# Kernel optimization log

Measured on AMD Instinct MI355X. Metric: run time of the kernel, lower is better.

## Reference

```python
import jax, jax.numpy as jnp
import numpy as np

N = 20000      # nodes
IN = 256       # in_dim
OUT = 128      # out_dim
S = 8          # num_sect
K = S + 1      # sectors + self branch
EP = 40000     # edges per sector


def setup_inputs() -> dict:
    key = jax.random.key(0)
    ks = jax.random.split(key, 10)
    x = jax.random.normal(ks[0], (N, IN), jnp.float32)
    rows = jax.random.randint(ks[1], (S, EP), 0, N)  # src (adj row)
    cols = jax.random.randint(ks[2], (S, EP), 0, N)  # dst (adj col)
    # degree norms (buffers derived from the graph, as in compute_norm)
    out_deg = np.bincount(np.asarray(rows).ravel(), minlength=N).astype(np.float32)
    in_deg = np.bincount(np.asarray(cols).ravel(), minlength=N).astype(np.float32)
    out_norm = jnp.asarray(np.clip(out_deg, 1.0, None) ** -0.5)[:, None]  # [N,1]
    in_norm = jnp.asarray(np.clip(in_deg, 1.0, None) ** -0.5)[:, None]    # [N,1]
    s = 0.05  # xavier-ish scale
    W_self = jax.random.normal(ks[3], (IN, OUT), jnp.float32) * s
    W_sect = jax.random.normal(ks[4], (S, IN, OUT), jnp.float32) * s
    WC = jax.random.normal(ks[5], (OUT, OUT), jnp.float32) * s
    WD = jax.random.normal(ks[6], (OUT, OUT), jnp.float32) * s
    gate_w = jax.random.normal(ks[7], (2 * K * OUT, 1), jnp.float32) * s
    gate_b = jnp.zeros((1,), jnp.float32)
    return {"x": x, "W_self": W_self, "W_sect": W_sect, "WC": WC, "WD": WD,
            "gate_w": gate_w, "gate_b": gate_b, "out_norm": out_norm,
            "in_norm": in_norm, "rows": rows, "cols": cols}


def reference(x, W_self, W_sect, WC, WD, gate_w, gate_b, out_norm, in_norm, rows, cols):
    n = x.shape[0]
    # --- forward_sector_agg (dropout is identity in eval / drop_rate=0) ---
    z_self = x @ W_self                                    # [N, OUT]
    H = jnp.einsum('ni,sio->sno', x, W_sect) * out_norm    # [S, N, OUT]
    def agg(h, r, c):  # sparse adj @ h : z[src] += h[dst]
        return jax.ops.segment_sum(h[c], r, num_segments=n)
    Z = jax.vmap(agg)(H, rows, cols)                       # [S, N, OUT]
    z = jnp.concatenate([z_self[None], Z], axis=0)         # [K, N, OUT]
    z = jnp.transpose(z, (1, 0, 2)) * in_norm[:, :, None]  # [N, K, OUT]
    # --- heter_sen_interaction ---
    zc = z @ WC                                            # [N, K, D]
    com = jnp.einsum('nkd,njd->nkj', zc, zc)
    ac = jax.nn.softmax(com, axis=2)
    z_com = jnp.einsum('nkj,njd->nkd', ac, zc).reshape(n, -1)
    zd = z @ WD
    sub = zd[:, :, None, :] - zd[:, None, :, :]            # [N, K, K, D]
    ds = jnp.einsum('nkd,nkjd->nkj', zd, sub)
    ad = jax.nn.softmax(ds, axis=2)
    z_dis = jnp.einsum('nkj,nkjd->nkd', ad, sub).reshape(n, -1)
    cat = jnp.concatenate([z_com, z_dis], axis=-1)         # [N, 2*K*D]
    beta = jax.nn.sigmoid(cat @ gate_w + gate_b)           # [N, 1]
    return beta * z_com + (1.0 - beta) * z_dis             # [N, K*D]
```

## Files before the change

kernel.cpp:

```cpp
#include <hip/hip_runtime.h>
#include <math.h>

#define N_NODES 20000
#define IN_DIM  256
#define OUT_DIM 128
#define S_SECT  8
#define K_BR    9
#define NK      (K_BR*OUT_DIM)
#define EP_EDGE 40000
#define N_EDGES (S_SECT*EP_EDGE)
#define N_BINS  (S_SECT*N_NODES)
#define SCAN_BLOCKS 160
#define M_ROWS  (N_NODES*K_BR)
#define ZP      136

typedef float v4f __attribute__((ext_vector_type(4)));
typedef short v8s __attribute__((ext_vector_type(8)));

__device__ inline unsigned short f2bf(float f) {
  union { float f; unsigned u; } v; v.f = f;
  unsigned r = v.u + 0x7fff + ((v.u >> 16) & 1);
  return (unsigned short)(r >> 16);
}
__device__ inline float bf2f(unsigned short h) {
  union { unsigned u; float f; } v; v.u = ((unsigned)h) << 16;
  return v.f;
}

__global__ __launch_bounds__(256) void k_prep_wt(
    const float* __restrict__ Wself, const float* __restrict__ Wsect,
    unsigned short* __restrict__ Wtg)
{
  const int id = blockIdx.x * 256 + threadIdx.x;
  if (id >= NK*IN_DIM) return;
  const int j = id >> 8, k = id & 255;
  float w;
  if (j < OUT_DIM) w = Wself[(size_t)k*OUT_DIM + j];
  else {
    const int s = (j - OUT_DIM) >> 7, c = (j - OUT_DIM) & 127;
    w = Wsect[(size_t)s*(IN_DIM*OUT_DIM) + (size_t)k*OUT_DIM + c];
  }
  Wtg[id] = f2bf(w);
}

__global__ __launch_bounds__(256) void k_prep_xbf(
    const float* __restrict__ x, unsigned short* __restrict__ xbf)
{
  const int id = blockIdx.x * 256 + threadIdx.x;
  if (id >= N_NODES*IN_DIM/4) return;
  const float4 v = ((const float4*)x)[id];
  uint2 o;
  o.x = (unsigned)f2bf(v.x) | ((unsigned)f2bf(v.y) << 16);
  o.y = (unsigned)f2bf(v.z) | ((unsigned)f2bf(v.w) << 16);
  ((uint2*)xbf)[id] = o;
}

__global__ __launch_bounds__(256, 4) void k_gemm_xw_mfma(
    const unsigned short* __restrict__ xbf, const unsigned short* __restrict__ Wtg,
    const float* __restrict__ outn, const float* __restrict__ inn,
    unsigned short* __restrict__ Hbuf, unsigned short* __restrict__ Zbufh)
{
  __shared__ unsigned short Bls[128*ZP];
  const int t = threadIdx.x;
  const int wave = t >> 6, lane = t & 63;
  const int mrow = lane & 15, quad = lane >> 4;
  const int m0 = blockIdx.x * 128 + wave * 32;
  const int jbase = blockIdx.y * 128;

  v4f acc[2][8];
  #pragma unroll
  for (int rb = 0; rb < 2; ++rb)
    #pragma unroll
    for (int jt = 0; jt < 8; ++jt) acc[rb][jt] = (v4f){0.f,0.f,0.f,0.f};

  for (int kh = 0; kh < 2; ++kh) {
    #pragma unroll
    for (int i = 0; i < 8; ++i) {
      const int idx = t + i*256;
      const int row = idx >> 4, c8 = idx & 15;
      *(uint4*)(Bls + row*ZP + c8*8) =
          *(const uint4*)(Wtg + (size_t)(jbase + row)*IN_DIM + kh*128 + c8*8);
    }
    v8s afr[2][4];
    #pragma unroll
    for (int rb = 0; rb < 2; ++rb) {
      const int r = m0 + rb*16 + mrow;
      const bool ok = (r < N_NODES);
      const unsigned short* src = xbf + (size_t)r*IN_DIM + kh*128 + quad*8;
      #pragma unroll
      for (int kq = 0; kq < 4; ++kq) {
        v8s f = {0,0,0,0,0,0,0,0};
        if (ok) f = *(const v8s*)(src + kq*32);
        afr[rb][kq] = f;
      }
    }
    __syncthreads();

    #pragma unroll
    for (int kq = 0; kq < 4; ++kq) {
      #pragma unroll
      for (int jt = 0; jt < 8; ++jt) {
        const v8s bf = *(const v8s*)(Bls + (jt*16 + mrow)*ZP + kq*32 + quad*8);
        acc[0][jt] = __builtin_amdgcn_mfma_f32_16x16x32_bf16(afr[0][kq], bf, acc[0][jt], 0, 0, 0);
        acc[1][jt] = __builtin_amdgcn_mfma_f32_16x16x32_bf16(afr[1][kq], bf, acc[1][jt], 0, 0, 0);
      }
    }
    __syncthreads();
  }

  if (blockIdx.y == 0) {
    #pragma unroll
    for (int rb = 0; rb < 2; ++rb)
      #pragma unroll
      for (int p = 0; p < 4; ++p) {
        const int R = m0 + rb*16 + quad*4 + p;
        if (R >= N_NODES) continue;
        const float iw = inn[R];
        #pragma unroll
        for (int jt = 0; jt < 8; ++jt)
          Zbufh[(size_t)R*NK + jt*16 + mrow] = f2bf(acc[rb][jt][p] * iw);
      }
  } else {
    const int s = blockIdx.y - 1;
    #pragma unroll
    for (int rb = 0; rb < 2; ++rb)
      #pragma unroll
      for (int p = 0; p < 4; ++p) {
        const int R = m0 + rb*16 + quad*4 + p;
        if (R >= N_NODES) continue;
        const float ow = outn[R];
        #pragma unroll
        for (int jt = 0; jt < 8; ++jt)
          Hbuf[((size_t)s*N_NODES + R)*OUT_DIM + jt*16 + mrow] = f2bf(acc[rb][jt][p] * ow);
      }
  }
}

__global__ __launch_bounds__(256) void k_count(
    const int* __restrict__ rows, int* __restrict__ cnt)
{
  const int id = blockIdx.x * 256 + threadIdx.x;
  if (id >= N_EDGES) return;
  const int s = id / EP_EDGE;
  atomicAdd(&cnt[s * N_NODES + rows[id]], 1);
}

__global__ __launch_bounds__(256) void k_scan1(
    const int* __restrict__ cnt, int* __restrict__ bsum)
{
  __shared__ int sh[256];
  const int t = threadIdx.x;
  const int base = blockIdx.x * 1000;
  int s = 0;
  if (t < 250) {
    const int i = base + t*4;
    s = cnt[i] + cnt[i+1] + cnt[i+2] + cnt[i+3];
  }
  sh[t] = s; __syncthreads();
  for (int off = 128; off > 0; off >>= 1) {
    if (t < off) sh[t] += sh[t + off];
    __syncthreads();
  }
  if (t == 0) bsum[blockIdx.x] = sh[0];
}

__global__ void k_scan2(const int* __restrict__ bsum, int* __restrict__ boff)
{
  if (threadIdx.x == 0) {
    int acc = 0;
    for (int b = 0; b < SCAN_BLOCKS; ++b) { boff[b] = acc; acc += bsum[b]; }
  }
}

__global__ __launch_bounds__(256) void k_scan3(
    const int* __restrict__ cnt, const int* __restrict__ boff,
    int* __restrict__ offs)
{
  __shared__ int sh[256];
  const int t = threadIdx.x;
  const int base = blockIdx.x * 1000;
  int v[4] = {0,0,0,0};
  int mySum = 0;
  if (t < 250) {
    const int i = base + t*4;
    v[0]=cnt[i]; v[1]=cnt[i+1]; v[2]=cnt[i+2]; v[3]=cnt[i+3];
    mySum = v[0]+v[1]+v[2]+v[3];
  }
  sh[t] = mySum; __syncthreads();
  for (int off = 1; off < 256; off <<= 1) {
    int add = (t >= off) ? sh[t - off] : 0;
    __syncthreads();
    sh[t] += add;
    __syncthreads();
  }
  if (t < 250) {
    int excl = boff[blockIdx.x] + sh[t] - mySum;
    const int i = base + t*4;
    offs[i]   = excl;           excl += v[0];
    offs[i+1] = excl;           excl += v[1];
    offs[i+2] = excl;           excl += v[2];
    offs[i+3] = excl;
  }
}

__global__ __launch_bounds__(256) void k_scatter(
    const int* __restrict__ rows, const int* __restrict__ cols,
    const int* __restrict__ offs, int* __restrict__ cur,
    int* __restrict__ eCol)
{
  const int id = blockIdx.x * 256 + threadIdx.x;
  if (id >= N_EDGES) return;
  const int s = id / EP_EDGE;
  const int bin = s * N_NODES + rows[id];
  const int pos = offs[bin] + atomicAdd(&cur[bin], 1);
  eCol[pos] = cols[id];
}

__global__ __launch_bounds__(256) void k_agg_csr(
    const unsigned short* __restrict__ Hbuf, const int* __restrict__ offs,
    const int* __restrict__ cnt, const int* __restrict__ eCol,
    const float* __restrict__ inn, unsigned short* __restrict__ Zbufh)
{
  const long long tid = (long long)blockIdx.x * 256 + threadIdx.x;
  const int group = (int)(tid >> 5);
  if (group >= N_BINS) return;
  const int lane = (int)(tid & 31);
  const int s = group / N_NODES;
  const int r = group - s * N_NODES;
  const int start = offs[group];
  const int n = cnt[group];
  float4 acc = {0.f, 0.f, 0.f, 0.f};
  for (int i = 0; i < n; ++i) {
    const int c = eCol[start + i];
    const uint2 h = *(const uint2*)(Hbuf + ((size_t)s*N_NODES + c)*OUT_DIM + lane*4);
    acc.x += bf2f((unsigned short)h.x);
    acc.y += bf2f((unsigned short)(h.x >> 16));
    acc.z += bf2f((unsigned short)h.y);
    acc.w += bf2f((unsigned short)(h.y >> 16));
  }
  const float w = inn[r];
  uint2 o;
  o.x = (unsigned)f2bf(acc.x * w) | ((unsigned)f2bf(acc.y * w) << 16);
  o.y = (unsigned)f2bf(acc.z * w) | ((unsigned)f2bf(acc.w * w) << 16);
  *(uint2*)(Zbufh + ((size_t)r*K_BR + 1 + s)*OUT_DIM + lane*4) = o;
}

__global__ __launch_bounds__(256) void k_prep_bt(
    const float* __restrict__ WC, const float* __restrict__ WD,
    unsigned short* __restrict__ Btg)
{
  const int id = blockIdx.x * 256 + threadIdx.x;
  const int n = id >> 7, k = id & 127;
  const float w = (n < OUT_DIM) ? WC[k*OUT_DIM + n] : WD[k*OUT_DIM + (n - OUT_DIM)];
  Btg[id] = f2bf(w);
}

__global__ __launch_bounds__(256, 4) void k_gemm_zcd(
    const unsigned short* __restrict__ Zbufh, const unsigned short* __restrict__ Btg,
    unsigned short* __restrict__ ZCD)
{
  __shared__ unsigned short Bls[128*ZP];
  const int t = threadIdx.x;
  const int wave = t >> 6, lane = t & 63;
  const int m0 = blockIdx.x * 128 + wave * 32;
  const int mrow = lane & 15, quad = lane >> 4;

  v8s afr[2][4];
  #pragma unroll
  for (int rb = 0; rb < 2; ++rb) {
    const int r = m0 + rb*16 + mrow;
    const bool ok = (r < M_ROWS);
    const unsigned short* src = Zbufh + (size_t)r*OUT_DIM + quad*8;
    #pragma unroll
    for (int kq = 0; kq < 4; ++kq) {
      v8s f = {0,0,0,0,0,0,0,0};
      if (ok) f = *(const v8s*)(src + kq*32);
      afr[rb][kq] = f;
    }
  }

  for (int jh = 0; jh < 2; ++jh) {
    #pragma unroll
    for (int i = 0; i < 8; ++i) {
      const int idx = t + i*256;
      const int row = idx >> 4, c8 = idx & 15;
      *(uint4*)(Bls + row*ZP + c8*8) =
          *(const uint4*)(Btg + (size_t)(jh*128 + row)*OUT_DIM + c8*8);
    }
    __syncthreads();

    v4f acc[2][8];
    #pragma unroll
    for (int rb = 0; rb < 2; ++rb)
      #pragma unroll
      for (int j = 0; j < 8; ++j) acc[rb][j] = (v4f){0.f,0.f,0.f,0.f};

    #pragma unroll
    for (int j = 0; j < 8; ++j) {
      const unsigned short* bp = Bls + (j*16 + mrow)*ZP + quad*8;
      #pragma unroll
      for (int kq = 0; kq < 4; ++kq) {
        const v8s bf = *(const v8s*)(bp + kq*32);
        acc[0][j] = __builtin_amdgcn_mfma_f32_16x16x32_bf16(afr[0][kq], bf, acc[0][j], 0, 0, 0);
        acc[1][j] = __builtin_amdgcn_mfma_f32_16x16x32_bf16(afr[1][kq], bf, acc[1][j], 0, 0, 0);
      }
    }

    unsigned short* Z = ZCD + (size_t)jh * N_NODES * NK;
    #pragma unroll
    for (int rb = 0; rb < 2; ++rb)
      #pragma unroll
      for (int p = 0; p < 4; ++p) {
        const int R = m0 + rb*16 + quad*4 + p;
        if (R >= M_ROWS) continue;
        const int node = R / 9, kk = R - node*9;
        const size_t base = (size_t)node*NK + kk*OUT_DIM;
        #pragma unroll
        for (int j = 0; j < 8; ++j)
          Z[base + j*16 + mrow] = f2bf(acc[rb][j][p]);
      }
    __syncthreads();
  }
}

__global__ __launch_bounds__(256) void k_interact3(
    const unsigned short* __restrict__ ZCD,
    const float* __restrict__ gw, const float* __restrict__ gb,
    float* __restrict__ out)
{
  __shared__ float graw[8][2][K_BR][10];
  __shared__ float gs[8][2][K_BR][10];
  __shared__ float redw[2][2];
  const int t  = threadIdx.x;
  const int n0 = blockIdx.x * 8;

  {
    const int wv = t >> 6, lane = t & 63;
    const int r = lane & 15, quad = lane >> 4;
    #pragma unroll
    for (int q = 0; q < 4; ++q) {
      const int idx = wv*4 + q;
      const int node = idx >> 1, mat = idx & 1;
      const unsigned short* src = ZCD + (size_t)mat*N_NODES*NK
                                  + (size_t)(n0+node)*NK + (size_t)r*OUT_DIM + quad*8;
      v8s frag[4];
      #pragma unroll
      for (int kq = 0; kq < 4; ++kq) {
        v8s f = {0,0,0,0,0,0,0,0};
        if (r < K_BR) f = *(const v8s*)(src + kq*32);
        frag[kq] = f;
      }
      v4f acc = {0.f,0.f,0.f,0.f};
      #pragma unroll
      for (int kq = 0; kq < 4; ++kq)
        acc = __builtin_amdgcn_mfma_f32_16x16x32_bf16(frag[kq], frag[kq], acc, 0, 0, 0);
      if (r < K_BR) {
        #pragma unroll
        for (int p = 0; p < 4; ++p) {
          const int m = quad*4 + p;
          if (m < K_BR) graw[node][mat][m][r] = acc[p];
        }
      }
    }
  }
  __syncthreads();

  if (t < 144) {
    const int node = t / 18;
    const int rem  = t - node*18;
    const int mat  = (rem >= 9) ? 1 : 0;
    const int k    = rem - mat*9;
    float v[9];
    if (mat == 0) {
      #pragma unroll
      for (int j = 0; j < 9; ++j) v[j] = graw[node][0][k][j];
    } else {
      const float gkk = graw[node][1][k][k];
      #pragma unroll
      for (int j = 0; j < 9; ++j) v[j] = gkk - graw[node][1][k][j];
    }
    float m = v[0];
    #pragma unroll
    for (int j = 1; j < 9; ++j) m = fmaxf(m, v[j]);
    float sum = 0.f;
    #pragma unroll
    for (int j = 0; j < 9; ++j) { v[j] = expf(v[j] - m); sum += v[j]; }
    const float inv = 1.f / sum;
    #pragma unroll
    for (int j = 0; j < 9; ++j) gs[node][mat][k][j] = v[j] * inv;
  }
  __syncthreads();

  const int half = t >> 7;
  const int d    = t & 127;
  const int wh   = (t >> 6) & 1;
  const int lane = t & 63;
  const float gbv = gb[0];
  float gwc[9], gwd[9];
  #pragma unroll
  for (int j = 0; j < 9; ++j) {
    gwc[j] = gw[j*OUT_DIM + d];
    gwd[j] = gw[NK + j*OUT_DIM + d];
  }

  for (int nn = 0; nn < 4; ++nn) {
    const int node = half*4 + nn;
    const unsigned short* zcp = ZCD + (size_t)(n0+node)*NK + d;
    const unsigned short* zdp = zcp + (size_t)N_NODES*NK;
    float zcj[9], zdj[9];
    #pragma unroll
    for (int j = 0; j < 9; ++j) {
      zcj[j] = bf2f(zcp[j*OUT_DIM]);
      zdj[j] = bf2f(zdp[j*OUT_DIM]);
    }
    float zcomK[9], zdisK[9];
    float gp = 0.f;
    #pragma unroll
    for (int k = 0; k < 9; ++k) {
      float zc = 0.f, ad = 0.f;
      #pragma unroll
      for (int j = 0; j < 9; ++j) {
        zc += gs[node][0][k][j] * zcj[j];
        ad += gs[node][1][k][j] * zdj[j];
      }
      zcomK[k] = zc;
      zdisK[k] = zdj[k] - ad;
      gp += zc * gwc[k] + zdisK[k] * gwd[k];
    }
    #pragma unroll
    for (int off = 32; off > 0; off >>= 1) gp += __shfl_down(gp, off, 64);
    if (lane == 0) redw[half][wh] = gp;
    __syncthreads();
    const float beta = 1.f / (1.f + expf(-(redw[half][0] + redw[half][1] + gbv)));
    #pragma unroll
    for (int k = 0; k < 9; ++k)
      out[(size_t)(n0+node)*NK + k*OUT_DIM + d] = beta*zcomK[k] + (1.f-beta)*zdisK[k];
    __syncthreads();
  }
}

extern "C" void kernel_launch(void* const* d_in, const int* in_sizes, int n_in,
                              void* d_out, int out_size, void* d_ws, size_t ws_size,
                              hipStream_t stream)
{
  const float* x     = (const float*)d_in[0];
  const float* Wself = (const float*)d_in[1];
  const float* Wsect = (const float*)d_in[2];
  const float* WC    = (const float*)d_in[3];
  const float* WD    = (const float*)d_in[4];
  const float* gw    = (const float*)d_in[5];
  const float* gb    = (const float*)d_in[6];
  const float* outn  = (const float*)d_in[7];
  const float* inn   = (const float*)d_in[8];
  const int*   rows  = (const int*)d_in[9];
  const int*   cols  = (const int*)d_in[10];
  float* out = (float*)d_out;

  char* p = (char*)d_ws;
  unsigned short* Hbuf  = (unsigned short*)p; p += (size_t)S_SECT*N_NODES*OUT_DIM*2;
  unsigned short* Zbufh = (unsigned short*)p; p += (size_t)M_ROWS*OUT_DIM*2;
  unsigned short* ZCD   = (unsigned short*)p; p += (size_t)2*N_NODES*NK*2;
  int* cnt    = (int*)p;                      p += (size_t)N_BINS*4;
  int* offs   = (int*)p;                      p += (size_t)N_BINS*4;
  int* cur    = (int*)p;                      p += (size_t)N_BINS*4;
  int* bsum   = (int*)p;                      p += 256*4;
  int* boff   = (int*)p;                      p += 256*4;
  int* eCol   = (int*)p;                      p += (size_t)N_EDGES*4;
  unsigned short* Btg = (unsigned short*)p;   p += 256*128*2;
  unsigned short* Wtg = (unsigned short*)p;   p += (size_t)NK*IN_DIM*2;
  unsigned short* xbf = (unsigned short*)p;   p += (size_t)N_NODES*IN_DIM*2;

  hipMemsetAsync(cnt, 0, (size_t)N_BINS*4, stream);
  hipMemsetAsync(cur, 0, (size_t)N_BINS*4, stream);

  k_prep_wt<<<(NK*IN_DIM + 255)/256, 256, 0, stream>>>(Wself, Wsect, Wtg);
  k_prep_bt<<<128, 256, 0, stream>>>(WC, WD, Btg);
  k_prep_xbf<<<(N_NODES*IN_DIM/4 + 255)/256, 256, 0, stream>>>(x, xbf);

  dim3 gA((N_NODES + 127)/128, K_BR);
  k_gemm_xw_mfma<<<gA, 256, 0, stream>>>(xbf, Wtg, outn, inn, Hbuf, Zbufh);

  const int eb = (N_EDGES + 255)/256;
  k_count  <<<eb, 256, 0, stream>>>(rows, cnt);
  k_scan1  <<<SCAN_BLOCKS, 256, 0, stream>>>(cnt, bsum);
  k_scan2  <<<1, 64, 0, stream>>>(bsum, boff);
  k_scan3  <<<SCAN_BLOCKS, 256, 0, stream>>>(cnt, boff, offs);
  k_scatter<<<eb, 256, 0, stream>>>(rows, cols, offs, cur, eCol);

  const int aggBlocks = (N_BINS*32 + 255)/256;
  k_agg_csr<<<aggBlocks, 256, 0, stream>>>(Hbuf, offs, cnt, eCol, inn, Zbufh);

  k_gemm_zcd<<<(M_ROWS + 127)/128, 256, 0, stream>>>(Zbufh, Btg, ZCD);

  k_interact3<<<N_NODES/8, 256, 0, stream>>>(ZCD, gw, gb, out);
}
```

Before: 323.2 us.

## Fuse prep kernels, convert x in-GEMM, and stage ZCD tiles in LDS for interaction

Merges the two weight-prep kernels into one launch and drops the separate x-to-bf16 kernel: the first GEMM now loads fp32 x directly and converts it in registers. The GEMM is retiled to 64 rows per block, with each block covering three 128-column output slices, so the A fragment is loaded once and reused. The interaction kernel saves the ZCD fragments it already loads into LDS and reads them from there, instead of reloading them from global memory. The cost is fewer blocks in the first GEMM, a larger LDS footprint in the interaction kernel (lower occupancy), and repeated Wtg tile loads per block.

```diff
diff --git a/kernel.cpp b/kernel.cpp
--- a/kernel.cpp
+++ b/kernel.cpp
@@ -13,6 +13,7 @@
 #define SCAN_BLOCKS 160
 #define M_ROWS  (N_NODES*K_BR)
 #define ZP      136
+#define TP      136
 
 typedef float v4f __attribute__((ext_vector_type(4)));
 typedef short v8s __attribute__((ext_vector_type(8)));
@@ -27,36 +28,33 @@
   return v.f;
 }
 
-__global__ __launch_bounds__(256) void k_prep_wt(
+__global__ __launch_bounds__(256) void k_prep(
     const float* __restrict__ Wself, const float* __restrict__ Wsect,
-    unsigned short* __restrict__ Wtg)
+    const float* __restrict__ WC, const float* __restrict__ WD,
+    unsigned short* __restrict__ Wtg, unsigned short* __restrict__ Btg)
 {
   const int id = blockIdx.x * 256 + threadIdx.x;
-  if (id >= NK*IN_DIM) return;
-  const int j = id >> 8, k = id & 255;
-  float w;
-  if (j < OUT_DIM) w = Wself[(size_t)k*OUT_DIM + j];
-  else {
-    const int s = (j - OUT_DIM) >> 7, c = (j - OUT_DIM) & 127;
-    w = Wsect[(size_t)s*(IN_DIM*OUT_DIM) + (size_t)k*OUT_DIM + c];
-  }
-  Wtg[id] = f2bf(w);
-}
-
-__global__ __launch_bounds__(256) void k_prep_xbf(
-    const float* __restrict__ x, unsigned short* __restrict__ xbf)
-{
-  const int id = blockIdx.x * 256 + threadIdx.x;
-  if (id >= N_NODES*IN_DIM/4) return;
-  const float4 v = ((const float4*)x)[id];
-  uint2 o;
-  o.x = (unsigned)f2bf(v.x) | ((unsigned)f2bf(v.y) << 16);
-  o.y = (unsigned)f2bf(v.z) | ((unsigned)f2bf(v.w) << 16);
-  ((uint2*)xbf)[id] = o;
+  if (id < NK*IN_DIM) {
+    const int j = id >> 8, k = id & 255;
+    float w;
+    if (j < OUT_DIM) w = Wself[(size_t)k*OUT_DIM + j];
+    else {
+      const int s = (j - OUT_DIM) >> 7, c = (j - OUT_DIM) & 127;
+      w = Wsect[(size_t)s*(IN_DIM*OUT_DIM) + (size_t)k*OUT_DIM + c];
+    }
+    Wtg[id] = f2bf(w);
+  } else {
+    const int id2 = id - NK*IN_DIM;
+    if (id2 < 256*128) {
+      const int n = id2 >> 7, k = id2 & 127;
+      const float w = (n < OUT_DIM) ? WC[k*OUT_DIM + n] : WD[k*OUT_DIM + (n - OUT_DIM)];
+      Btg[id2] = f2bf(w);
+    }
+  }
 }
 
 __global__ __launch_bounds__(256, 4) void k_gemm_xw_mfma(
-    const unsigned short* __restrict__ xbf, const unsigned short* __restrict__ Wtg,
+    const float* __restrict__ x, const unsigned short* __restrict__ Wtg,
     const float* __restrict__ outn, const float* __restrict__ inn,
     unsigned short* __restrict__ Hbuf, unsigned short* __restrict__ Zbufh)
 {
@@ -64,75 +62,79 @@
   const int t = threadIdx.x;
   const int wave = t >> 6, lane = t & 63;
   const int mrow = lane & 15, quad = lane >> 4;
-  const int m0 = blockIdx.x * 128 + wave * 32;
-  const int jbase = blockIdx.y * 128;
-
-  v4f acc[2][8];
-  #pragma unroll
-  for (int rb = 0; rb < 2; ++rb)
-    #pragma unroll
-    for (int jt = 0; jt < 8; ++jt) acc[rb][jt] = (v4f){0.f,0.f,0.f,0.f};
-
-  for (int kh = 0; kh < 2; ++kh) {
-    #pragma unroll
-    for (int i = 0; i < 8; ++i) {
-      const int idx = t + i*256;
-      const int row = idx >> 4, c8 = idx & 15;
-      *(uint4*)(Bls + row*ZP + c8*8) =
-          *(const uint4*)(Wtg + (size_t)(jbase + row)*IN_DIM + kh*128 + c8*8);
-    }
-    v8s afr[2][4];
-    #pragma unroll
-    for (int rb = 0; rb < 2; ++rb) {
-      const int r = m0 + rb*16 + mrow;
-      const bool ok = (r < N_NODES);
-      const unsigned short* src = xbf + (size_t)r*IN_DIM + kh*128 + quad*8;
+  const int m0 = blockIdx.x * 64 + wave * 16;
+
+  v8s afr[8];
+  {
+    const int r = m0 + mrow;
+    const bool ok = (r < N_NODES);
+    const float* src = x + (size_t)r*IN_DIM + quad*8;
+    #pragma unroll
+    for (int kq = 0; kq < 8; ++kq) {
+      float4 a0 = {0.f,0.f,0.f,0.f}, a1 = {0.f,0.f,0.f,0.f};
+      if (ok) {
+        a0 = *(const float4*)(src + kq*32);
+        a1 = *(const float4*)(src + kq*32 + 4);
+      }
+      v8s f;
+      f[0] = (short)f2bf(a0.x); f[1] = (short)f2bf(a0.y);
+      f[2] = (short)f2bf(a0.z); f[3] = (short)f2bf(a0.w);
+      f[4] = (short)f2bf(a1.x); f[5] = (short)f2bf(a1.y);
+      f[6] = (short)f2bf(a1.z); f[7] = (short)f2bf(a1.w);
+      afr[kq] = f;
+    }
+  }
+
+  for (int jj = 0; jj < 3; ++jj) {
+    const int jb = blockIdx.y * 3 + jj;
+
+    v4f acc[8];
+    #pragma unroll
+    for (int jt = 0; jt < 8; ++jt) acc[jt] = (v4f){0.f,0.f,0.f,0.f};
+
+    for (int kh = 0; kh < 2; ++kh) {
+      #pragma unroll
+      for (int i = 0; i < 8; ++i) {
+        const int idx = t + i*256;
+        const int row = idx >> 4, c8 = idx & 15;
+        *(uint4*)(Bls + row*ZP + c8*8) =
+            *(const uint4*)(Wtg + (size_t)(jb*128 + row)*IN_DIM + kh*128 + c8*8);
+      }
+      __syncthreads();
+
       #pragma unroll
       for (int kq = 0; kq < 4; ++kq) {
-        v8s f = {0,0,0,0,0,0,0,0};
-        if (ok) f = *(const v8s*)(src + kq*32);
-        afr[rb][kq] = f;
-      }
-    }
-    __syncthreads();
-
-    #pragma unroll
-    for (int kq = 0; kq < 4; ++kq) {
-      #pragma unroll
-      for (int jt = 0; jt < 8; ++jt) {
-        const v8s bf = *(const v8s*)(Bls + (jt*16 + mrow)*ZP + kq*32 + quad*8);
-        acc[0][jt] = __builtin_amdgcn_mfma_f32_16x16x32_bf16(afr[0][kq], bf, acc[0][jt], 0, 0, 0);
-        acc[1][jt] = __builtin_amdgcn_mfma_f32_16x16x32_bf16(afr[1][kq], bf, acc[1][jt], 0, 0, 0);
-      }
-    }
-    __syncthreads();
-  }
-
-  if (blockIdx.y == 0) {
-    #pragma unroll
-    for (int rb = 0; rb < 2; ++rb)
+        #pragma unroll
+        for (int jt = 0; jt < 8; ++jt) {
+          const v8s bf = *(const v8s*)(Bls + (jt*16 + mrow)*ZP + kq*32 + quad*8);
+          acc[jt] = __builtin_amdgcn_mfma_f32_16x16x32_bf16(afr[kh*4 + kq], bf, acc[jt], 0, 0, 0);
+        }
+      }
+      __syncthreads();
+    }
+
+    if (jb == 0) {
       #pragma unroll
       for (int p = 0; p < 4; ++p) {
-        const int R = m0 + rb*16 + quad*4 + p;
+        const int R = m0 + quad*4 + p;
         if (R >= N_NODES) continue;
         const float iw = inn[R];
         #pragma unroll
         for (int jt = 0; jt < 8; ++jt)
-          Zbufh[(size_t)R*NK + jt*16 + mrow] = f2bf(acc[rb][jt][p] * iw);
-      }
-  } else {
-    const int s = blockIdx.y - 1;
-    #pragma unroll
-    for (int rb = 0; rb < 2; ++rb)
+          Zbufh[(size_t)R*NK + jt*16 + mrow] = f2bf(acc[jt][p] * iw);
+      }
+    } else {
+      const int s = jb - 1;
       #pragma unroll
       for (int p = 0; p < 4; ++p) {
-        const int R = m0 + rb*16 + quad*4 + p;
+        const int R = m0 + quad*4 + p;
         if (R >= N_NODES) continue;
         const float ow = outn[R];
         #pragma unroll
         for (int jt = 0; jt < 8; ++jt)
-          Hbuf[((size_t)s*N_NODES + R)*OUT_DIM + jt*16 + mrow] = f2bf(acc[rb][jt][p] * ow);
-      }
+          Hbuf[((size_t)s*N_NODES + R)*OUT_DIM + jt*16 + mrow] = f2bf(acc[jt][p] * ow);
+      }
+    }
   }
 }
 
@@ -245,16 +247,6 @@
   *(uint2*)(Zbufh + ((size_t)r*K_BR + 1 + s)*OUT_DIM + lane*4) = o;
 }
 
-__global__ __launch_bounds__(256) void k_prep_bt(
-    const float* __restrict__ WC, const float* __restrict__ WD,
-    unsigned short* __restrict__ Btg)
-{
-  const int id = blockIdx.x * 256 + threadIdx.x;
-  const int n = id >> 7, k = id & 127;
-  const float w = (n < OUT_DIM) ? WC[k*OUT_DIM + n] : WD[k*OUT_DIM + (n - OUT_DIM)];
-  Btg[id] = f2bf(w);
-}
-
 __global__ __launch_bounds__(256, 4) void k_gemm_zcd(
     const unsigned short* __restrict__ Zbufh, const unsigned short* __restrict__ Btg,
     unsigned short* __restrict__ ZCD)
@@ -323,11 +315,12 @@
   }
 }
 
-__global__ __launch_bounds__(256) void k_interact3(
+__global__ __launch_bounds__(256) void k_interact4(
     const unsigned short* __restrict__ ZCD,
     const float* __restrict__ gw, const float* __restrict__ gb,
     float* __restrict__ out)
 {
+  __shared__ unsigned short tls[8][2][9*TP];
   __shared__ float graw[8][2][K_BR][10];
   __shared__ float gs[8][2][K_BR][10];
   __shared__ float redw[2][2];
@@ -349,6 +342,11 @@
         v8s f = {0,0,0,0,0,0,0,0};
         if (r < K_BR) f = *(const v8s*)(src + kq*32);
         frag[kq] = f;
+      }
+      if (r < K_BR) {
+        #pragma unroll
+        for (int kq = 0; kq < 4; ++kq)
+          *(v8s*)&tls[node][mat][r*TP + kq*32 + quad*8] = frag[kq];
       }
       v4f acc = {0.f,0.f,0.f,0.f};
       #pragma unroll
@@ -405,13 +403,11 @@
 
   for (int nn = 0; nn < 4; ++nn) {
     const int node = half*4 + nn;
-    const unsigned short* zcp = ZCD + (size_t)(n0+node)*NK + d;
-    const unsigned short* zdp = zcp + (size_t)N_NODES*NK;
     float zcj[9], zdj[9];
     #pragma unroll
     for (int j = 0; j < 9; ++j) {
-      zcj[j] = bf2f(zcp[j*OUT_DIM]);
-      zdj[j] = bf2f(zdp[j*OUT_DIM]);
+      zcj[j] = bf2f(tls[node][0][j*TP + d]);
+      zdj[j] = bf2f(tls[node][1][j*TP + d]);
     }
     float zcomK[9], zdisK[9];
     float gp = 0.f;
@@ -468,17 +464,14 @@
   int* eCol   = (int*)p;                      p += (size_t)N_EDGES*4;
   unsigned short* Btg = (unsigned short*)p;   p += 256*128*2;
   unsigned short* Wtg = (unsigned short*)p;   p += (size_t)NK*IN_DIM*2;
-  unsigned short* xbf = (unsigned short*)p;   p += (size_t)N_NODES*IN_DIM*2;
 
   hipMemsetAsync(cnt, 0, (size_t)N_BINS*4, stream);
   hipMemsetAsync(cur, 0, (size_t)N_BINS*4, stream);
 
-  k_prep_wt<<<(NK*IN_DIM + 255)/256, 256, 0, stream>>>(Wself, Wsect, Wtg);
-  k_prep_bt<<<128, 256, 0, stream>>>(WC, WD, Btg);
-  k_prep_xbf<<<(N_NODES*IN_DIM/4 + 255)/256, 256, 0, stream>>>(x, xbf);
-
-  dim3 gA((N_NODES + 127)/128, K_BR);
-  k_gemm_xw_mfma<<<gA, 256, 0, stream>>>(xbf, Wtg, outn, inn, Hbuf, Zbufh);
+  k_prep<<<(NK*IN_DIM + 256*128 + 255)/256, 256, 0, stream>>>(Wself, Wsect, WC, WD, Wtg, Btg);
+
+  dim3 gA((N_NODES + 63)/64, 3);
+  k_gemm_xw_mfma<<<gA, 256, 0, stream>>>(x, Wtg, outn, inn, Hbuf, Zbufh);
 
   const int eb = (N_EDGES + 255)/256;
   k_count  <<<eb, 256, 0, stream>>>(rows, cnt);
@@ -492,5 +485,5 @@
 
   k_gemm_zcd<<<(M_ROWS + 127)/128, 256, 0, stream>>>(Zbufh, Btg, ZCD);
 
-  k_interact3<<<N_NODES/8, 256, 0, stream>>>(ZCD, gw, gb, out);
-}
+  k_interact4<<<N_NODES/8, 256, 0, stream>>>(ZCD, gw, gb, out);
+}
```

After: 320.0 us. No clear change (-1.0%).
